# Performance work log

Hardware: AMD Instinct MI355X
Metric: run time of the kernel (lower is better)

Reference implementation:

```python
import jax, jax.numpy as jnp
import numpy as np

C = 256          # channels
K = 7            # kernel_size
GC = 16          # group_channels (hardcoded in module)
G = C // GC      # groups = 16
RED = 4          # reduction_ratio
PAD = (K - 1) // 2
EPS = 1e-5


def _bn(x, gamma, beta, mean, var):
    # inference-mode BatchNorm2d over channel dim (axis=1)
    inv = gamma / jnp.sqrt(var + EPS)
    return x * inv[None, :, None, None] + (beta - mean * inv)[None, :, None, None]


def setup_inputs() -> dict:
    key = jax.random.key(0)
    ks = jax.random.split(key, 8)
    cm = C // RED  # 64
    x = jax.random.normal(ks[0], (4, C, 64, 64), dtype=jnp.float32)
    w1 = jax.random.normal(ks[1], (cm, C), dtype=jnp.float32) * (1.0 / np.sqrt(C))
    bn1_gamma = jnp.abs(jax.random.normal(ks[2], (cm,), dtype=jnp.float32)) + 0.5
    bn1_beta = jax.random.normal(ks[3], (cm,), dtype=jnp.float32) * 0.1
    bn1_mean = jnp.zeros((cm,), jnp.float32)
    bn1_var = jnp.ones((cm,), jnp.float32)
    w2 = jax.random.normal(ks[4], (K * K * G, cm), dtype=jnp.float32) * (1.0 / np.sqrt(cm))
    b2 = jax.random.normal(ks[5], (K * K * G,), dtype=jnp.float32) * 0.1
    bn2_gamma = jnp.abs(jax.random.normal(ks[6], (C,), dtype=jnp.float32)) + 0.5
    bn2_beta = jax.random.normal(ks[7], (C,), dtype=jnp.float32) * 0.1
    bn2_mean = jnp.zeros((C,), jnp.float32)
    bn2_var = jnp.ones((C,), jnp.float32)
    return {"x": x, "w1": w1, "bn1_gamma": bn1_gamma, "bn1_beta": bn1_beta,
            "bn1_mean": bn1_mean, "bn1_var": bn1_var, "w2": w2, "b2": b2,
            "bn2_gamma": bn2_gamma, "bn2_beta": bn2_beta,
            "bn2_mean": bn2_mean, "bn2_var": bn2_var}


def reference(x, w1, bn1_gamma, bn1_beta, bn1_mean, bn1_var,
              w2, b2, bn2_gamma, bn2_beta, bn2_mean, bn2_var):
    b, c, h, w = x.shape
    # weight branch: 1x1 conv (no bias) -> BN -> ReLU -> 1x1 conv (bias)
    t = jnp.einsum('oc,bchw->bohw', w1, x)
    t = jax.nn.relu(_bn(t, bn1_gamma, bn1_beta, bn1_mean, bn1_var))
    wgt = jnp.einsum('oc,bchw->bohw', w2, t) + b2[None, :, None, None]
    wgt = wgt.reshape(b, G, K * K, h, w)  # per-pixel kernel per group
    # unfold x: extract KxK patches (stride 1, pad PAD), torch ordering:
    # channel slowest, kernel row, kernel col fastest
    x_pad = jnp.pad(x, ((0, 0), (0, 0), (PAD, PAD), (PAD, PAD)))
    patches = jnp.stack([x_pad[:, :, i:i + h, j:j + w]
                         for i in range(K) for j in range(K)], axis=2)  # (b,c,K2,h,w)
    patches = patches.reshape(b, G, GC, K * K, h, w)
    out = jnp.einsum('bgckhw,bgkhw->bgchw', patches, wgt).reshape(b, c, h, w)
    return jax.nn.relu(_bn(out, bn2_gamma, bn2_beta, bn2_mean, bn2_var))
```

## Files before the change

### kernel.cpp

```cpp
#include <hip/hip_runtime.h>

#define BN 4
#define C 256
#define H 64
#define W 64
#define CM 64
#define G 16
#define GC 16
#define KS 7
#define K2 49
#define PADD 3
#define EPSV 1e-5f

#define TS 16
#define HALO_R 22
#define HROWF 32
#define HSLOTF (HALO_R * HROWF)

#define W1T_OFF 0
#define B2P_OFF (W1T_OFF + C*CM)
#define S1_OFF  (B2P_OFF + G*64)
#define B1_OFF  (S1_OFF + CM)
#define S2_OFF  (B1_OFF + CM)
#define B2C_OFF (S2_OFF + C)
#define ZERO_OFF (B2C_OFF + C)
#define ABF_OFF (ZERO_OFF + 16)
#define TBF_OFF (ABF_OFF + 32768)

typedef __attribute__((ext_vector_type(8))) short bf16x8;
typedef __attribute__((ext_vector_type(4))) float f32x4;

__device__ __forceinline__ uint f2bf_rne(float f) {
  uint u = __float_as_uint(f);
  return (u + 0x7fffu + ((u >> 16) & 1u)) >> 16;
}

__device__ __forceinline__ void gload_lds4(const float* g, float* l) {
  __builtin_amdgcn_global_load_lds(
      (const __attribute__((address_space(1))) void*)g,
      (__attribute__((address_space(3))) void*)l, 4, 0, 0);
}

__global__ __launch_bounds__(256) void prep_kernel(
    const float* __restrict__ w1, const float* __restrict__ w2,
    const float* __restrict__ b2,
    const float* __restrict__ g1, const float* __restrict__ be1,
    const float* __restrict__ m1, const float* __restrict__ v1,
    const float* __restrict__ g2, const float* __restrict__ be2,
    const float* __restrict__ m2, const float* __restrict__ v2,
    float* __restrict__ ws) {
  int tid = blockIdx.x * 256 + threadIdx.x;
  int nthr = gridDim.x * 256;
  for (int i = tid; i < CM * C; i += nthr) {
    int o = i / C, c = i - o * C;
    ws[W1T_OFF + c * CM + o] = w1[i];
  }
  {
    ushort* abf = (ushort*)(ws + ABF_OFF);
    for (int i = tid; i < G * 4 * 2 * 64 * 8; i += nthr) {
      int j = i & 7, lane = (i >> 3) & 63, ks = (i >> 9) & 1;
      int mt = (i >> 10) & 3, g = (i >> 12) & 15;
      int m = mt * 16 + (lane & 15);
      int o = ks * 32 + ((lane >> 4) << 3) + j;
      float v = (m < K2) ? w2[(g * K2 + m) * CM + o] : 0.f;
      abf[i] = (ushort)f2bf_rne(v);
    }
  }
  for (int i = tid; i < G * 64; i += nthr) {
    int g = i >> 6, k = i & 63;
    ws[B2P_OFF + i] = (k < K2) ? b2[g * K2 + k] : 0.f;
  }
  if (tid < CM) {
    float inv = g1[tid] * rsqrtf(v1[tid] + EPSV);
    ws[S1_OFF + tid] = inv;
    ws[B1_OFF + tid] = be1[tid] - m1[tid] * inv;
  }
  if (tid < C) {
    float inv = g2[tid] * rsqrtf(v2[tid] + EPSV);
    ws[S2_OFF + tid] = inv;
    ws[B2C_OFF + tid] = be2[tid] - m2[tid] * inv;
  }
  if (tid < 16) ws[ZERO_OFF + tid] = 0.f;
}

__global__ __launch_bounds__(256) void t_kernel(
    const float* __restrict__ x, float* __restrict__ ws) {
  __shared__ float part[4][32][64];
  int p = threadIdx.x & 63;
  int q = __builtin_amdgcn_readfirstlane(threadIdx.x >> 6);
  int y = blockIdx.x, b = blockIdx.y, oh = blockIdx.z;
  const float* __restrict__ w1T = ws + W1T_OFF + oh * 32;

  float acc[32];
#pragma unroll
  for (int o = 0; o < 32; ++o) acc[o] = 0.f;
  const float* __restrict__ xrow = x + (((size_t)b * C + q * 64) * H + y) * W;
#pragma unroll 2
  for (int cc = 0; cc < 64; ++cc) {
    float xv = xrow[(size_t)cc * H * W + p];
    const float* __restrict__ wr = w1T + (q * 64 + cc) * CM;
#pragma unroll
    for (int o = 0; o < 32; ++o) acc[o] = fmaf(wr[o], xv, acc[o]);
  }
#pragma unroll
  for (int o = 0; o < 32; ++o) part[q][o][p] = acc[o];
  __syncthreads();

  int tile = (y >> 4) * 4 + (p >> 4);
  int pix = (y & 15) * 16 + (p & 15);
  const float* __restrict__ s1 = ws + S1_OFF + oh * 32;
  const float* __restrict__ b1 = ws + B1_OFF + oh * 32;
  float fv[8];
#pragma unroll
  for (int i = 0; i < 8; ++i) {
    int o = q * 8 + i;
    float s = part[0][o][p] + part[1][o][p] + part[2][o][p] + part[3][o][p];
    fv[i] = fmaxf(fmaf(s, s1[o], b1[o]), 0.f);
  }
  uint4 pk;
  pk.x = f2bf_rne(fv[0]) | (f2bf_rne(fv[1]) << 16);
  pk.y = f2bf_rne(fv[2]) | (f2bf_rne(fv[3]) << 16);
  pk.z = f2bf_rne(fv[4]) | (f2bf_rne(fv[5]) << 16);
  pk.w = f2bf_rne(fv[6]) | (f2bf_rne(fv[7]) << 16);
  ushort* tbf = (ushort*)(ws + TBF_OFF);
  size_t idx = (((size_t)(b * 16 + tile) * 256 + pix) * 64) + oh * 32 + q * 8;
  *(uint4*)(tbf + idx) = pk;
}

__global__ __launch_bounds__(256, 1) void inv_kernel(
    const float* __restrict__ x, const float* __restrict__ ws,
    float* __restrict__ out) {
  __shared__ uint wgt_u[256 * 32];
  __shared__ float xh[G * HSLOTF];

  int tid = threadIdx.x;
  int lane = tid & 63;
  int wv = __builtin_amdgcn_readfirstlane(tid >> 6);
  int c16 = lane & 15, q = lane >> 4;
  int tile = blockIdx.x, g = blockIdx.y, b = blockIdx.z;
  int ty = (tile >> 2) * TS, tx = (tile & 3) * TS;

  const ushort* abf = (const ushort*)(ws + ABF_OFF);
  const ushort* tbf = (const ushort*)(ws + TBF_OFF);

  bf16x8 afr[4][2], bfr[4][2];
  f32x4 bias[4];
#pragma unroll
  for (int mt = 0; mt < 4; ++mt) {
#pragma unroll
    for (int ks = 0; ks < 2; ++ks)
      afr[mt][ks] = *(const bf16x8*)(abf + (((g * 8 + mt * 2 + ks) * 64 + lane) * 8));
    bias[mt] = *(const f32x4*)(ws + B2P_OFF + g * 64 + mt * 16 + q * 4);
  }
#pragma unroll
  for (int nt = 0; nt < 4; ++nt) {
    int pix = wv * 64 + nt * 16 + c16;
#pragma unroll
    for (int ks = 0; ks < 2; ++ks)
      bfr[nt][ks] = *(const bf16x8*)(
          tbf + (((size_t)(b * 16 + tile) * 256 + pix) * 64 + ks * 32 + q * 8));
  }

  {
    const float* zsrc = ws + ZERO_OFF;
    const float* xg = x + ((size_t)b * C + g * GC) * (H * W);
#pragma unroll
    for (int j = 0; j < 4; ++j) {
      int ch = wv * 4 + j;
      const float* xc = xg + (size_t)ch * (H * W);
      float* ldst = &xh[ch * HSLOTF];
#pragma unroll
      for (int t2 = 0; t2 < 11; ++t2) {
        int f = t2 * 64 + lane;
        int row = f >> 5;
        int cp = (f >> 2) & 7, sub = f & 3;
        int col = (((cp ^ (row & 7)) << 2)) + sub;
        int gy = ty + row - PADD, gx = tx + col - PADD;
        bool v = (col < HALO_R) && ((unsigned)gy < H) && ((unsigned)gx < W);
        const float* s = v ? (xc + gy * W + gx) : zsrc;
        gload_lds4(s, ldst + t2 * 64);
      }
    }
  }

  f32x4 acc[4][4];
#pragma unroll
  for (int nt = 0; nt < 4; ++nt)
#pragma unroll
    for (int mt = 0; mt < 4; ++mt) acc[nt][mt] = bias[mt];
#pragma unroll
  for (int ks = 0; ks < 2; ++ks)
#pragma unroll
    for (int nt = 0; nt < 4; ++nt)
#pragma unroll
      for (int mt = 0; mt < 4; ++mt)
        acc[nt][mt] = __builtin_amdgcn_mfma_f32_16x16x32_bf16(
            afr[mt][ks], bfr[nt][ks], acc[nt][mt], 0, 0, 0);

#pragma unroll
  for (int nt = 0; nt < 4; ++nt) {
    int pix = wv * 64 + nt * 16 + c16;
    int swz = ((pix >> 4) << 2) + ((pix >> 2) & 3);
    uint* wrow = &wgt_u[pix * 32];
#pragma unroll
    for (int mt = 0; mt < 4; ++mt) {
      uint lo = f2bf_rne(acc[nt][mt].x) | (f2bf_rne(acc[nt][mt].y) << 16);
      uint hi = f2bf_rne(acc[nt][mt].z) | (f2bf_rne(acc[nt][mt].w) << 16);
      int i0 = mt * 8 + q * 2;
      wrow[(i0 + swz) & 31] = lo;
      wrow[(i0 + 1 + swz) & 31] = hi;
    }
  }

  __syncthreads();

  int py = lane >> 2;
  int px0 = (lane & 3) << 2;
  int P = px0 >> 2;

  uint wp[4][25];
#pragma unroll
  for (int i = 0; i < 4; ++i) {
    int p = py * 16 + px0 + i;
    int swz = ((p >> 4) << 2) + ((p >> 2) & 3);
    const uint* wrow = &wgt_u[p * 32];
#pragma unroll
    for (int t = 0; t < 25; ++t) wp[i][t] = wrow[(t + swz) & 31];
  }

  const float* s2 = ws + S2_OFF + g * GC;
  const float* b2c = ws + B2C_OFF + g * GC;

#pragma unroll
  for (int jc = 0; jc < 4; ++jc) {
    int ch = wv * 4 + jc;
    const float* hch = &xh[ch * HSLOTF];
    float a0 = 0.f, a1 = 0.f, a2 = 0.f, a3 = 0.f;
#pragma unroll
    for (int di = 0; di < KS; ++di) {
      int row = py + di;
      int r7 = row & 7;
      f32x4 h0 = *(const f32x4*)&hch[row * HROWF + (((P + 0) ^ r7) << 2)];
      f32x4 h1 = *(const f32x4*)&hch[row * HROWF + (((P + 1) ^ r7) << 2)];
      f32x4 h2 = *(const f32x4*)&hch[row * HROWF + (((P + 2) ^ r7) << 2)];
      float rw[12] = {h0.x, h0.y, h0.z, h0.w, h1.x, h1.y, h1.z, h1.w,
                      h2.x, h2.y, h2.z, h2.w};
#pragma unroll
      for (int dj = 0; dj < KS; ++dj) {
        int k = di * KS + dj;
        uint m0 = wp[0][k >> 1], m1 = wp[1][k >> 1];
        uint m2v = wp[2][k >> 1], m3 = wp[3][k >> 1];
        float w0, w1, w2f, w3;
        if (k & 1) {
          w0 = __uint_as_float(m0 & 0xffff0000u);
          w1 = __uint_as_float(m1 & 0xffff0000u);
          w2f = __uint_as_float(m2v & 0xffff0000u);
          w3 = __uint_as_float(m3 & 0xffff0000u);
        } else {
          w0 = __uint_as_float(m0 << 16);
          w1 = __uint_as_float(m1 << 16);
          w2f = __uint_as_float(m2v << 16);
          w3 = __uint_as_float(m3 << 16);
        }
        a0 = fmaf(rw[0 + dj], w0, a0);
        a1 = fmaf(rw[1 + dj], w1, a1);
        a2 = fmaf(rw[2 + dj], w2f, a2);
        a3 = fmaf(rw[3 + dj], w3, a3);
      }
    }
    float sc = s2[ch], bc = b2c[ch];
    float4 o4;
    o4.x = fmaxf(fmaf(a0, sc, bc), 0.f);
    o4.y = fmaxf(fmaf(a1, sc, bc), 0.f);
    o4.z = fmaxf(fmaf(a2, sc, bc), 0.f);
    o4.w = fmaxf(fmaf(a3, sc, bc), 0.f);
    *(float4*)(out + (((size_t)b * C + g * GC + ch) * H + ty + py) * W + tx + px0) = o4;
  }
}

extern "C" void kernel_launch(void* const* d_in, const int* in_sizes, int n_in,
                              void* d_out, int out_size, void* d_ws, size_t ws_size,
                              hipStream_t stream) {
  const float* x   = (const float*)d_in[0];
  const float* w1  = (const float*)d_in[1];
  const float* g1  = (const float*)d_in[2];
  const float* be1 = (const float*)d_in[3];
  const float* m1  = (const float*)d_in[4];
  const float* v1  = (const float*)d_in[5];
  const float* w2  = (const float*)d_in[6];
  const float* b2  = (const float*)d_in[7];
  const float* g2  = (const float*)d_in[8];
  const float* be2 = (const float*)d_in[9];
  const float* m2  = (const float*)d_in[10];
  const float* v2  = (const float*)d_in[11];
  float* outp = (float*)d_out;
  float* ws = (float*)d_ws;

  prep_kernel<<<dim3(64), dim3(256), 0, stream>>>(w1, w2, b2, g1, be1, m1, v1,
                                                  g2, be2, m2, v2, ws);
  t_kernel<<<dim3(H, BN, 2), dim3(256), 0, stream>>>(x, ws);
  inv_kernel<<<dim3(16, G, BN), dim3(256), 0, stream>>>(x, ws, outp);
}
```

Measured before the change: 57.88 us.

## Double-buffer halo staging across channel phases and raise occupancy in inv_kernel

Halo loads now go into a two-slot LDS buffer of four channels each and are issued in stages, so loading the next pair of channels overlaps the involution FMAs on the current pair. The per-pixel weight table is moved to a k-major [25][256] layout read as uint4 per kernel row instead of 100 registers per thread, and threads are remapped so each wave covers all pixels for one channel lane. LDS footprint and register pressure drop, which allows three blocks per CU via launch bounds. The hand-written vmcnt waits and barriers must match the exact number of issued loads, so they are fragile.

```diff
diff --git a/kernel.cpp b/kernel.cpp
--- a/kernel.cpp
+++ b/kernel.cpp
@@ -15,7 +15,7 @@
 #define TS 16
 #define HALO_R 22
 #define HROWF 32
-#define HSLOTF (HALO_R * HROWF)
+#define HSLOTP 712
 
 #define W1T_OFF 0
 #define B2P_OFF (W1T_OFF + C*CM)
@@ -40,6 +40,18 @@
       (const __attribute__((address_space(1))) void*)g,
       (__attribute__((address_space(3))) void*)l, 4, 0, 0);
 }
+
+#define WAITBAR(N) do {                                            \
+    asm volatile("s_waitcnt vmcnt(" #N ") lgkmcnt(0)" ::: "memory"); \
+    __builtin_amdgcn_s_barrier();                                  \
+    __builtin_amdgcn_sched_barrier(0);                             \
+  } while (0)
+
+#define BARRIER_ONLY() do {                                        \
+    asm volatile("s_waitcnt lgkmcnt(0)" ::: "memory");             \
+    __builtin_amdgcn_s_barrier();                                  \
+    __builtin_amdgcn_sched_barrier(0);                             \
+  } while (0)
 
 __global__ __launch_bounds__(256) void prep_kernel(
     const float* __restrict__ w1, const float* __restrict__ w2,
@@ -127,29 +139,38 @@
   *(uint4*)(tbf + idx) = pk;
 }
 
-__global__ __launch_bounds__(256, 1) void inv_kernel(
+__global__ __launch_bounds__(256, 3) void inv_kernel(
     const float* __restrict__ x, const float* __restrict__ ws,
     float* __restrict__ out) {
-  __shared__ uint wgt_u[256 * 32];
-  __shared__ float xh[G * HSLOTF];
+  __shared__ uint wgt_u[25][256];
+  __shared__ float xh[2][4][HSLOTP];
 
   int tid = threadIdx.x;
   int lane = tid & 63;
   int wv = __builtin_amdgcn_readfirstlane(tid >> 6);
   int c16 = lane & 15, q = lane >> 4;
+  int py = tid >> 4, chl = (tid >> 2) & 3, pq = tid & 3;
+  int px0 = pq << 2;
   int tile = blockIdx.x, g = blockIdx.y, b = blockIdx.z;
   int ty = (tile >> 2) * TS, tx = (tile & 3) * TS;
 
   const ushort* abf = (const ushort*)(ws + ABF_OFF);
   const ushort* tbf = (const ushort*)(ws + TBF_OFF);
 
+  float scv[4], bcv[4];
+#pragma unroll
+  for (int p = 0; p < 4; ++p) {
+    scv[p] = ws[S2_OFF + g * GC + p * 4 + chl];
+    bcv[p] = ws[B2C_OFF + g * GC + p * 4 + chl];
+  }
+
   bf16x8 afr[4][2], bfr[4][2];
   f32x4 bias[4];
 #pragma unroll
   for (int mt = 0; mt < 4; ++mt) {
 #pragma unroll
     for (int ks = 0; ks < 2; ++ks)
-      afr[mt][ks] = *(const bf16x8*)(abf + (((g * 8 + mt * 2 + ks) * 64 + lane) * 8));
+      afr[mt][ks] = *(const bf16x8*)(abf + ((g * 8 + mt * 2 + ks) * 64 + lane) * 8);
     bias[mt] = *(const f32x4*)(ws + B2P_OFF + g * 64 + mt * 16 + q * 4);
   }
 #pragma unroll
@@ -161,121 +182,107 @@
           tbf + (((size_t)(b * 16 + tile) * 256 + pix) * 64 + ks * 32 + q * 8));
   }
 
-  {
-    const float* zsrc = ws + ZERO_OFF;
-    const float* xg = x + ((size_t)b * C + g * GC) * (H * W);
-#pragma unroll
-    for (int j = 0; j < 4; ++j) {
-      int ch = wv * 4 + j;
-      const float* xc = xg + (size_t)ch * (H * W);
-      float* ldst = &xh[ch * HSLOTF];
-#pragma unroll
-      for (int t2 = 0; t2 < 11; ++t2) {
-        int f = t2 * 64 + lane;
-        int row = f >> 5;
-        int cp = (f >> 2) & 7, sub = f & 3;
-        int col = (((cp ^ (row & 7)) << 2)) + sub;
-        int gy = ty + row - PADD, gx = tx + col - PADD;
-        bool v = (col < HALO_R) && ((unsigned)gy < H) && ((unsigned)gx < W);
-        const float* s = v ? (xc + gy * W + gx) : zsrc;
-        gload_lds4(s, ldst + t2 * 64);
+  uint hmask = 0;
+  int hofs[11];
+#pragma unroll
+  for (int t2 = 0; t2 < 11; ++t2) {
+    int f = t2 * 64 + lane;
+    int row = f >> 5, cp = (f >> 2) & 7, sub = f & 3;
+    int s8 = (row + 3 * (row >> 3)) & 7;
+    int col = ((cp ^ s8) << 2) + sub;
+    int gy = ty + row - PADD, gx = tx + col - PADD;
+    bool v = (col < HALO_R) && ((unsigned)gy < H) && ((unsigned)gx < W);
+    hmask |= (uint)v << t2;
+    hofs[t2] = gy * W + gx;
+  }
+  const float* zsrc = ws + ZERO_OFF;
+  const float* xg = x + ((size_t)b * C + g * GC) * (H * W);
+
+#define STAGE(CH, BUF) do {                                         \
+    const float* xc_ = xg + (size_t)(CH) * (H * W);                 \
+    float* dst_ = &xh[BUF][(CH) & 3][0];                            \
+    _Pragma("unroll")                                               \
+    for (int t2 = 0; t2 < 11; ++t2) {                               \
+      const float* s_ = ((hmask >> t2) & 1u) ? (xc_ + hofs[t2]) : zsrc; \
+      gload_lds4(s_, dst_ + t2 * 64);                               \
+    }                                                               \
+  } while (0)
+
+  STAGE(wv, 0);
+  STAGE(4 + wv, 1);
+
+#pragma unroll
+  for (int nt = 0; nt < 4; ++nt) {
+    f32x4 a[4];
+#pragma unroll
+    for (int mt = 0; mt < 4; ++mt) a[mt] = bias[mt];
+#pragma unroll
+    for (int ks = 0; ks < 2; ++ks)
+#pragma unroll
+      for (int mt = 0; mt < 4; ++mt)
+        a[mt] = __builtin_amdgcn_mfma_f32_16x16x32_bf16(afr[mt][ks], bfr[nt][ks],
+                                                        a[mt], 0, 0, 0);
+    int pix = wv * 64 + nt * 16 + c16;
+#pragma unroll
+    for (int mt = 0; mt < 4; ++mt) {
+      uint lo = f2bf_rne(a[mt][0]) | (f2bf_rne(a[mt][1]) << 16);
+      uint hi = f2bf_rne(a[mt][2]) | (f2bf_rne(a[mt][3]) << 16);
+      int j0v = mt * 8 + q * 2;
+      if (j0v < 25) wgt_u[j0v][pix] = lo;
+      if (j0v + 1 < 25) wgt_u[j0v + 1][pix] = hi;
+    }
+  }
+
+  auto phase = [&](int bufI, int p) {
+    f32x4 acc = {0.f, 0.f, 0.f, 0.f};
+#pragma unroll
+    for (int di = 0; di < KS; ++di) {
+      const int j0 = (di * 7) >> 1;
+      uint4 wq[4];
+#pragma unroll
+      for (int m = 0; m < 4; ++m)
+        wq[m] = *(const uint4*)&wgt_u[j0 + m][py * 16 + px0];
+      int row = py + di;
+      int s8 = (row + 3 * (row >> 3)) & 7;
+      const float* hb = &xh[bufI][chl][row * HROWF];
+      f32x4 h0 = *(const f32x4*)&hb[((pq + 0) ^ s8) << 2];
+      f32x4 h1 = *(const f32x4*)&hb[((pq + 1) ^ s8) << 2];
+      f32x4 h2 = *(const f32x4*)&hb[((pq + 2) ^ s8) << 2];
+      float rw[12] = {h0[0], h0[1], h0[2], h0[3], h1[0], h1[1],
+                      h1[2], h1[3], h2[0], h2[1], h2[2], h2[3]};
+#pragma unroll
+      for (int dj = 0; dj < KS; ++dj) {
+        const int k = di * 7 + dj, m = (k >> 1) - j0, hf = k & 1;
+#pragma unroll
+        for (int i = 0; i < 4; ++i) {
+          uint u = (&wq[m].x)[i];
+          float wf = __uint_as_float(hf ? (u & 0xffff0000u) : (u << 16));
+          acc[i] = fmaf(rw[i + dj], wf, acc[i]);
+        }
       }
     }
-  }
-
-  f32x4 acc[4][4];
-#pragma unroll
-  for (int nt = 0; nt < 4; ++nt)
-#pragma unroll
-    for (int mt = 0; mt < 4; ++mt) acc[nt][mt] = bias[mt];
-#pragma unroll
-  for (int ks = 0; ks < 2; ++ks)
-#pragma unroll
-    for (int nt = 0; nt < 4; ++nt)
-#pragma unroll
-      for (int mt = 0; mt < 4; ++mt)
-        acc[nt][mt] = __builtin_amdgcn_mfma_f32_16x16x32_bf16(
-            afr[mt][ks], bfr[nt][ks], acc[nt][mt], 0, 0, 0);
-
-#pragma unroll
-  for (int nt = 0; nt < 4; ++nt) {
-    int pix = wv * 64 + nt * 16 + c16;
-    int swz = ((pix >> 4) << 2) + ((pix >> 2) & 3);
-    uint* wrow = &wgt_u[pix * 32];
-#pragma unroll
-    for (int mt = 0; mt < 4; ++mt) {
-      uint lo = f2bf_rne(acc[nt][mt].x) | (f2bf_rne(acc[nt][mt].y) << 16);
-      uint hi = f2bf_rne(acc[nt][mt].z) | (f2bf_rne(acc[nt][mt].w) << 16);
-      int i0 = mt * 8 + q * 2;
-      wrow[(i0 + swz) & 31] = lo;
-      wrow[(i0 + 1 + swz) & 31] = hi;
-    }
-  }
-
-  __syncthreads();
-
-  int py = lane >> 2;
-  int px0 = (lane & 3) << 2;
-  int P = px0 >> 2;
-
-  uint wp[4][25];
-#pragma unroll
-  for (int i = 0; i < 4; ++i) {
-    int p = py * 16 + px0 + i;
-    int swz = ((p >> 4) << 2) + ((p >> 2) & 3);
-    const uint* wrow = &wgt_u[p * 32];
-#pragma unroll
-    for (int t = 0; t < 25; ++t) wp[i][t] = wrow[(t + swz) & 31];
-  }
-
-  const float* s2 = ws + S2_OFF + g * GC;
-  const float* b2c = ws + B2C_OFF + g * GC;
-
-#pragma unroll
-  for (int jc = 0; jc < 4; ++jc) {
-    int ch = wv * 4 + jc;
-    const float* hch = &xh[ch * HSLOTF];
-    float a0 = 0.f, a1 = 0.f, a2 = 0.f, a3 = 0.f;
-#pragma unroll
-    for (int di = 0; di < KS; ++di) {
-      int row = py + di;
-      int r7 = row & 7;
-      f32x4 h0 = *(const f32x4*)&hch[row * HROWF + (((P + 0) ^ r7) << 2)];
-      f32x4 h1 = *(const f32x4*)&hch[row * HROWF + (((P + 1) ^ r7) << 2)];
-      f32x4 h2 = *(const f32x4*)&hch[row * HROWF + (((P + 2) ^ r7) << 2)];
-      float rw[12] = {h0.x, h0.y, h0.z, h0.w, h1.x, h1.y, h1.z, h1.w,
-                      h2.x, h2.y, h2.z, h2.w};
-#pragma unroll
-      for (int dj = 0; dj < KS; ++dj) {
-        int k = di * KS + dj;
-        uint m0 = wp[0][k >> 1], m1 = wp[1][k >> 1];
-        uint m2v = wp[2][k >> 1], m3 = wp[3][k >> 1];
-        float w0, w1, w2f, w3;
-        if (k & 1) {
-          w0 = __uint_as_float(m0 & 0xffff0000u);
-          w1 = __uint_as_float(m1 & 0xffff0000u);
-          w2f = __uint_as_float(m2v & 0xffff0000u);
-          w3 = __uint_as_float(m3 & 0xffff0000u);
-        } else {
-          w0 = __uint_as_float(m0 << 16);
-          w1 = __uint_as_float(m1 << 16);
-          w2f = __uint_as_float(m2v << 16);
-          w3 = __uint_as_float(m3 << 16);
-        }
-        a0 = fmaf(rw[0 + dj], w0, a0);
-        a1 = fmaf(rw[1 + dj], w1, a1);
-        a2 = fmaf(rw[2 + dj], w2f, a2);
-        a3 = fmaf(rw[3 + dj], w3, a3);
-      }
-    }
-    float sc = s2[ch], bc = b2c[ch];
+    int ch = p * 4 + chl;
     float4 o4;
-    o4.x = fmaxf(fmaf(a0, sc, bc), 0.f);
-    o4.y = fmaxf(fmaf(a1, sc, bc), 0.f);
-    o4.z = fmaxf(fmaf(a2, sc, bc), 0.f);
-    o4.w = fmaxf(fmaf(a3, sc, bc), 0.f);
+    o4.x = fmaxf(fmaf(acc[0], scv[p], bcv[p]), 0.f);
+    o4.y = fmaxf(fmaf(acc[1], scv[p], bcv[p]), 0.f);
+    o4.z = fmaxf(fmaf(acc[2], scv[p], bcv[p]), 0.f);
+    o4.w = fmaxf(fmaf(acc[3], scv[p], bcv[p]), 0.f);
     *(float4*)(out + (((size_t)b * C + g * GC + ch) * H + ty + py) * W + tx + px0) = o4;
-  }
+  };
+
+  WAITBAR(11);
+  phase(0, 0);
+  BARRIER_ONLY();
+  STAGE(8 + wv, 0);
+  WAITBAR(12);
+  phase(1, 1);
+  BARRIER_ONLY();
+  STAGE(12 + wv, 1);
+  WAITBAR(12);
+  phase(0, 2);
+  WAITBAR(1);
+  phase(1, 3);
+#undef STAGE
 }
 
 extern "C" void kernel_launch(void* const* d_in, const int* in_sizes, int n_in,
```

Measured after the change: 47.61 us. 1.22x faster.
